# Kernel optimization log

Hardware: AMD Instinct MI355X
Metric: run time of the kernel (lower is better)

The kernel has to match this reference:

```python
import jax, jax.numpy as jnp
import numpy as np
from math import sqrt

DIM = 1024
RANK = 64
B, T = 4, 4096

def _xavier(key, shape):
    fan_in, fan_out = shape[1], shape[0]
    limit = sqrt(6.0 / (fan_in + fan_out))
    return jax.random.uniform(key, shape, jnp.float32, -limit, limit)

def setup_inputs() -> dict:
    key = jax.random.key(0)
    kx, kq, kk, kv = jax.random.split(key, 4)
    return {
        "x": jax.random.normal(kx, (B, T, DIM), jnp.float32),
        "Q": _xavier(kq, (RANK, DIM)),
        "K": _xavier(kk, (RANK, DIM)),
        "VO": _xavier(kv, (DIM, DIM)),
    }

def reference(x, Q, K, VO):
    dim = x.shape[-1]
    # low-rank projections: [b, t, r]
    xq = jnp.einsum('btd,rd->btr', x, Q)
    xk = jnp.einsum('bue,re->bur', x, K)
    scores = jnp.einsum('btr,bur->btu', xq, xk) / sqrt(dim)
    attn = jax.nn.softmax(scores, axis=2)
    # attn @ x @ VO: contract with VO first (cheap [b,u,d]@[d,e]) then attn
    return jnp.einsum('btu,bue->bte', attn, x @ VO)
```

## Files before the change

kernel.cpp:

```cpp
#include <hip/hip_runtime.h>
#include <hip/hip_bf16.h>

#define BATCH 4
#define SEQ   4096
#define DIM   1024
#define RANK  64

typedef __attribute__((ext_vector_type(8))) short short8;
typedef __attribute__((ext_vector_type(4))) short short4v;
typedef __attribute__((ext_vector_type(4))) float f32x4;

#define MFMA16(a,b,c) __builtin_amdgcn_mfma_f32_16x16x32_bf16((a),(b),(c),0,0,0)

#define XQ_OFF 0
#define XK_OFF (BATCH*SEQ*RANK)
#define VT_OFF (2*BATCH*SEQ*RANK)
#define VT_END (VT_OFF + BATCH*DIM*SEQ)
#define P_OFF  ((size_t)VT_END)
#define P_LEN  ((size_t)BATCH*SEQ*SEQ)

__device__ __forceinline__ short f2b(float f) {
    __hip_bfloat16 h = __float2bfloat16(f);
    short s; __builtin_memcpy(&s, &h, sizeof(short));
    return s;
}
__device__ __forceinline__ float b2f(short s) {
    __hip_bfloat16 h; __builtin_memcpy(&h, &s, sizeof(short));
    return __bfloat162float(h);
}
__device__ __forceinline__ short8 cvt8(const float* __restrict__ p) {
    const float4 f0 = *reinterpret_cast<const float4*>(p);
    const float4 f1 = *reinterpret_cast<const float4*>(p + 4);
    short8 r;
    r[0]=f2b(f0.x); r[1]=f2b(f0.y); r[2]=f2b(f0.z); r[3]=f2b(f0.w);
    r[4]=f2b(f1.x); r[5]=f2b(f1.y); r[6]=f2b(f1.z); r[7]=f2b(f1.w);
    return r;
}
__device__ __forceinline__ void gld16(const short* g, short* l) {
    __builtin_amdgcn_global_load_lds(
        (const __attribute__((address_space(1))) void*)g,
        (__attribute__((address_space(3))) void*)l, 16, 0, 0);
}

__global__ __launch_bounds__(256) void lr_cvt(const float* __restrict__ x,
                                              const float* __restrict__ VO,
                                              const float* __restrict__ Qw,
                                              const float* __restrict__ Kw,
                                              short* __restrict__ xb,
                                              short* __restrict__ VOt,
                                              short* __restrict__ Wb)
{
    const int bid = blockIdx.x, tid = threadIdx.x;
    if (bid < 8192) {
        const size_t base = ((size_t)bid*256 + tid)*8;
        *reinterpret_cast<short8*>(xb + base) = cvt8(x + base);
    } else if (bid < 8448) {
        __shared__ short tr[64*68];
        const int bb = bid - 8192;
        const int dt = bb >> 4, et = bb & 15;
        const int d0 = dt*64, e0 = et*64;
        const int ein = tid & 63, din = tid >> 6;
        #pragma unroll
        for (int j = 0; j < 16; ++j) {
            const int dl = din + j*4;
            tr[ein*68 + dl] = f2b(VO[(size_t)(d0 + dl)*DIM + e0 + ein]);
        }
        __syncthreads();
        const int or_ = tid >> 4, oc = (tid & 15)*4;
        #pragma unroll
        for (int j = 0; j < 4; ++j) {
            const int el = or_ + j*16;
            short4v v;
            v[0]=tr[el*68+oc]; v[1]=tr[el*68+oc+1];
            v[2]=tr[el*68+oc+2]; v[3]=tr[el*68+oc+3];
            *reinterpret_cast<short4v*>(VOt + (size_t)(e0+el)*DIM + d0 + oc) = v;
        }
    } else {
        const int gid = (bid - 8448)*256 + tid;
        const int row = gid >> 7, c8 = (gid & 127)*8;
        const float* src = (row < 64 ? Qw + (size_t)row*DIM
                                     : Kw + (size_t)(row-64)*DIM) + c8;
        *reinterpret_cast<short8*>(Wb + (size_t)row*DIM + c8) = cvt8(src);
    }
}

__global__ __launch_bounds__(256, 4) void lr_proj2(const short* __restrict__ xb,
                                                   const short* __restrict__ Wb,
                                                   short* __restrict__ ws)
{
    __shared__ __align__(16) short As[128*64];
    __shared__ __align__(16) short Bs[128*64];
    const int t0 = blockIdx.x*128;
    const int tid = threadIdx.x, lane = tid & 63, w = tid >> 6;
    const int l15 = lane & 15, g = lane >> 4;
    const int wr = w >> 1, wc = w & 1;
    const short* Ab = xb + (size_t)t0*DIM;
    const short* Bb = Wb;
    const int srow = lane >> 3;
    const int skc  = ((lane & 7) ^ srow)*8;
    const int rx = l15 & 7;

    f32x4 acc[4][4] = {};
    #pragma unroll
    for (int j = 0; j < 4; ++j) {
        const int ch = 4*w + j, row = ch*8 + srow;
        gld16(Ab + (size_t)row*DIM + skc, &As[ch*512]);
        gld16(Bb + (size_t)row*DIM + skc, &Bs[ch*512]);
    }
    for (int kt = 0; kt < 16; ++kt) {
        __syncthreads();
        #pragma unroll
        for (int ks = 0; ks < 2; ++ks) {
            short8 af[4], bfr[4];
            #pragma unroll
            for (int mr = 0; mr < 4; ++mr)
                af[mr] = *reinterpret_cast<const short8*>(
                    &As[(wr*64 + mr*16 + l15)*64 + ((ks*4 + g) ^ rx)*8]);
            #pragma unroll
            for (int ct = 0; ct < 4; ++ct)
                bfr[ct] = *reinterpret_cast<const short8*>(
                    &Bs[(wc*64 + ct*16 + l15)*64 + ((ks*4 + g) ^ rx)*8]);
            #pragma unroll
            for (int mr = 0; mr < 4; ++mr)
                #pragma unroll
                for (int ct = 0; ct < 4; ++ct)
                    acc[mr][ct] = MFMA16(af[mr], bfr[ct], acc[mr][ct]);
        }
        if (kt < 15) {
            __syncthreads();
            const int k0 = (kt + 1)*64;
            #pragma unroll
            for (int j = 0; j < 4; ++j) {
                const int ch = 4*w + j, row = ch*8 + srow;
                gld16(Ab + (size_t)row*DIM + k0 + skc, &As[ch*512]);
                gld16(Bb + (size_t)row*DIM + k0 + skc, &Bs[ch*512]);
            }
        }
    }
    short* xqp = ws + XQ_OFF;
    short* xkp = ws + XK_OFF;
    #pragma unroll
    for (int mr = 0; mr < 4; ++mr)
        #pragma unroll
        for (int rr = 0; rr < 4; ++rr) {
            const int t = t0 + wr*64 + mr*16 + g*4 + rr;
            #pragma unroll
            for (int ct = 0; ct < 4; ++ct) {
                const int r = wc*64 + ct*16 + l15;
                const short v = f2b(acc[mr][ct][rr]);
                if (r < RANK) xqp[(size_t)t*RANK + r] = v;
                else          xkp[(size_t)t*RANK + r - RANK] = v;
            }
        }
}

__global__ __launch_bounds__(256, 4) void lr_vgemm2(const short* __restrict__ VOt,
                                                    const short* __restrict__ xb,
                                                    short* __restrict__ vT)
{
    __shared__ __align__(16) short As[128*64];
    __shared__ __align__(16) short Bs[128*64];
    const int i = blockIdx.x;
    const int etile = i & 7, j = i >> 3;
    const int ut = j & 31, b = j >> 5;
    const int e0 = etile*128, u0 = ut*128;
    const int tid = threadIdx.x, lane = tid & 63, w = tid >> 6;
    const int l15 = lane & 15, g = lane >> 4;
    const int wr = w >> 1, wc = w & 1;
    const short* Ab = VOt + (size_t)e0*DIM;
    const short* Bb = xb + ((size_t)(b*SEQ) + u0)*DIM;
    const int srow = lane >> 3;
    const int skc  = ((lane & 7) ^ srow)*8;
    const int rx = l15 & 7;

    f32x4 acc[4][4] = {};
    #pragma unroll
    for (int jj = 0; jj < 4; ++jj) {
        const int ch = 4*w + jj, row = ch*8 + srow;
        gld16(Ab + (size_t)row*DIM + skc, &As[ch*512]);
        gld16(Bb + (size_t)row*DIM + skc, &Bs[ch*512]);
    }
    for (int kt = 0; kt < 16; ++kt) {
        __syncthreads();
        #pragma unroll
        for (int ks = 0; ks < 2; ++ks) {
            short8 af[4], bfr[4];
            #pragma unroll
            for (int mr = 0; mr < 4; ++mr)
                af[mr] = *reinterpret_cast<const short8*>(
                    &As[(wr*64 + mr*16 + l15)*64 + ((ks*4 + g) ^ rx)*8]);
            #pragma unroll
            for (int ct = 0; ct < 4; ++ct)
                bfr[ct] = *reinterpret_cast<const short8*>(
                    &Bs[(wc*64 + ct*16 + l15)*64 + ((ks*4 + g) ^ rx)*8]);
            #pragma unroll
            for (int mr = 0; mr < 4; ++mr)
                #pragma unroll
                for (int ct = 0; ct < 4; ++ct)
                    acc[mr][ct] = MFMA16(af[mr], bfr[ct], acc[mr][ct]);
        }
        if (kt < 15) {
            __syncthreads();
            const int k0 = (kt + 1)*64;
            #pragma unroll
            for (int jj = 0; jj < 4; ++jj) {
                const int ch = 4*w + jj, row = ch*8 + srow;
                gld16(Ab + (size_t)row*DIM + k0 + skc, &As[ch*512]);
                gld16(Bb + (size_t)row*DIM + k0 + skc, &Bs[ch*512]);
            }
        }
    }
    #pragma unroll
    for (int mr = 0; mr < 4; ++mr)
        #pragma unroll
        for (int rr = 0; rr < 4; ++rr) {
            const int e = e0 + wr*64 + mr*16 + g*4 + rr;
            short* orow = vT + ((size_t)(b*DIM) + e)*SEQ + u0 + wc*64;
            #pragma unroll
            for (int ct = 0; ct < 4; ++ct)
                orow[ct*16 + l15] = f2b(acc[mr][ct][rr]);
        }
}

__global__ __launch_bounds__(256, 4) void lr_pexp(const short* __restrict__ ws,
                                                  short* __restrict__ P,
                                                  float* __restrict__ ps)
{
    __shared__ __align__(16) short ptile[128*136];
    __shared__ float sred[4][128];
    const int i = blockIdx.x;
    const int qt = i >> 5, ut = i & 31;
    const int b = qt >> 5;
    const int tid = threadIdx.x, lane = tid & 63, w = tid >> 6;
    const int l15 = lane & 15, g = lane >> 4;
    const float cl = 0.045084220f;
    const int q0 = qt*128;

    const short* xqb = ws + XQ_OFF + (size_t)q0*RANK;
    const short* xkb = ws + XK_OFF + ((size_t)(b*SEQ) + ut*128)*RANK;

    f32x4 acc[2][8] = {};
    #pragma unroll
    for (int ks = 0; ks < 2; ++ks) {
        short8 ak[2], bq[8];
        #pragma unroll
        for (int mr = 0; mr < 2; ++mr)
            ak[mr] = *reinterpret_cast<const short8*>(
                xkb + (size_t)(32*w + mr*16 + l15)*RANK + ks*32 + g*8);
        #pragma unroll
        for (int ct = 0; ct < 8; ++ct)
            bq[ct] = *reinterpret_cast<const short8*>(
                xqb + (size_t)(ct*16 + l15)*RANK + ks*32 + g*8);
        #pragma unroll
        for (int mr = 0; mr < 2; ++mr)
            #pragma unroll
            for (int ct = 0; ct < 8; ++ct)
                acc[mr][ct] = MFMA16(ak[mr], bq[ct], acc[mr][ct]);
    }
    float s[8] = {0.f,0.f,0.f,0.f,0.f,0.f,0.f,0.f};
    #pragma unroll
    for (int mr = 0; mr < 2; ++mr)
        #pragma unroll
        for (int ct = 0; ct < 8; ++ct) {
            short4v pk;
            #pragma unroll
            for (int r = 0; r < 4; ++r) {
                const short pb = f2b(__builtin_amdgcn_exp2f(acc[mr][ct][r]*cl));
                pk[r] = pb;
                s[ct] += b2f(pb);
            }
            *reinterpret_cast<short4v*>(
                &ptile[(ct*16 + l15)*136 + 32*w + mr*16 + g*4]) = pk;
        }
    #pragma unroll
    for (int ct = 0; ct < 8; ++ct) {
        s[ct] += __shfl_xor(s[ct], 16);
        s[ct] += __shfl_xor(s[ct], 32);
    }
    if (g == 0) {
        #pragma unroll
        for (int ct = 0; ct < 8; ++ct) sred[w][ct*16 + l15] = s[ct];
    }
    __syncthreads();
    #pragma unroll
    for (int j = 0; j < 8; ++j) {
        const int id = tid + 256*j;
        const int row = id >> 4, seg = id & 15;
        const uint4 v = *reinterpret_cast<const uint4*>(&ptile[row*136 + seg*8]);
        *reinterpret_cast<uint4*>(
            P + (size_t)(q0 + row)*SEQ + ut*128 + seg*8) = v;
    }
    if (tid < 128)
        ps[(size_t)(q0 + tid)*32 + ut] =
            sred[0][tid] + sred[1][tid] + sred[2][tid] + sred[3][tid];
}

__global__ __launch_bounds__(256) void lr_psum(const float* __restrict__ ps,
                                               float* __restrict__ linv)
{
    const int gq = blockIdx.x*256 + threadIdx.x;
    const float* p = ps + (size_t)gq*32;
    float s = 0.f;
    #pragma unroll
    for (int j = 0; j < 32; ++j) s += p[j];
    linv[gq] = 1.0f / s;
}

__global__ __launch_bounds__(256, 4) void lr_pv(const short* __restrict__ P,
                                                const short* __restrict__ vT,
                                                const float* __restrict__ linv,
                                                float* __restrict__ out)
{
    __shared__ __align__(16) short As[128*64];
    __shared__ __align__(16) short Bs[128*64];
    const int i = blockIdx.x;
    const int qlo = i & 7, j = i >> 3;
    const int nt = j & 7, qhi = j >> 3;
    const int qt = qhi*8 + qlo;
    const int q0 = qt*128, d0 = nt*128, b = qt >> 5;
    const int tid = threadIdx.x, lane = tid & 63, w = tid >> 6;
    const int l15 = lane & 15, g = lane >> 4;
    const int wr = w >> 1, wc = w & 1;

    const short* Ab = P + (size_t)q0*SEQ;
    const short* Bb = vT + ((size_t)(b*DIM) + d0)*SEQ;
    const int srow = lane >> 3;
    const int skc  = ((lane & 7) ^ srow)*8;
    const int rx = l15 & 7;

    f32x4 acc[4][4] = {};
    #pragma unroll
    for (int jj = 0; jj < 4; ++jj) {
        const int ch = 4*w + jj, row = ch*8 + srow;
        gld16(Ab + (size_t)row*SEQ + skc, &As[ch*512]);
        gld16(Bb + (size_t)row*SEQ + skc, &Bs[ch*512]);
    }
    for (int kt = 0; kt < 64; ++kt) {
        __syncthreads();
        #pragma unroll
        for (int ks = 0; ks < 2; ++ks) {
            short8 af[4], bfr[4];
            #pragma unroll
            for (int mr = 0; mr < 4; ++mr)
                af[mr] = *reinterpret_cast<const short8*>(
                    &As[(wr*64 + mr*16 + l15)*64 + ((ks*4 + g) ^ rx)*8]);
            #pragma unroll
            for (int ct = 0; ct < 4; ++ct)
                bfr[ct] = *reinterpret_cast<const short8*>(
                    &Bs[(wc*64 + ct*16 + l15)*64 + ((ks*4 + g) ^ rx)*8]);
            #pragma unroll
            for (int mr = 0; mr < 4; ++mr)
                #pragma unroll
                for (int ct = 0; ct < 4; ++ct)
                    acc[mr][ct] = MFMA16(af[mr], bfr[ct], acc[mr][ct]);
        }
        if (kt < 63) {
            __syncthreads();
            const int k0 = (kt + 1)*64;
            #pragma unroll
            for (int jj = 0; jj < 4; ++jj) {
                const int ch = 4*w + jj, row = ch*8 + srow;
                gld16(Ab + (size_t)row*SEQ + k0 + skc, &As[ch*512]);
                gld16(Bb + (size_t)row*SEQ + k0 + skc, &Bs[ch*512]);
            }
        }
    }
    #pragma unroll
    for (int mr = 0; mr < 4; ++mr)
        #pragma unroll
        for (int rr = 0; rr < 4; ++rr) {
            const int q = q0 + wr*64 + mr*16 + g*4 + rr;
            const float sc = linv[q];
            float* rp = out + (size_t)q*DIM + d0 + wc*64;
            #pragma unroll
            for (int ct = 0; ct < 4; ++ct)
                rp[ct*16 + l15] = acc[mr][ct][rr]*sc;
        }
}

__global__ __launch_bounds__(256) void lr_proj(const float* __restrict__ x,
                                               const float* __restrict__ Qw,
                                               const float* __restrict__ Kw,
                                               short* __restrict__ ws)
{
    __shared__ __align__(16) short ldsB[64*40];
    const int i = blockIdx.x;
    const int ttile = i & 63, b = i >> 6;
    const int tid = threadIdx.x, lane = tid & 63, w = tid >> 6;
    const int l15 = lane & 15, g = lane >> 4;
    const int t0 = ttile * 64;

    f32x4 acc[2][4] = {};
    for (int e0 = 0; e0 < DIM; e0 += 32) {
        const int tr = tid >> 2, seg = tid & 3;
        const float* px = x + (size_t)(b*SEQ + t0 + tr)*DIM + e0 + seg*8;
        const float4 f0 = *reinterpret_cast<const float4*>(px);
        const float4 f1 = *reinterpret_cast<const float4*>(px + 4);
        __syncthreads();
        {
            short* d = &ldsB[tr*40 + seg*8];
            d[0]=f2b(f0.x); d[1]=f2b(f0.y); d[2]=f2b(f0.z); d[3]=f2b(f0.w);
            d[4]=f2b(f1.x); d[5]=f2b(f1.y); d[6]=f2b(f1.z); d[7]=f2b(f1.w);
        }
        __syncthreads();
        #pragma unroll
        for (int mr = 0; mr < 2; ++mr) {
            const int r = 32*w + mr*16 + l15;
            const float* wp = (r < RANK ? Qw + (size_t)r*DIM
                                        : Kw + (size_t)(r - RANK)*DIM) + e0 + g*8;
            const short8 a = cvt8(wp);
            #pragma unroll
            for (int ct = 0; ct < 4; ++ct) {
                const short8 bb = *reinterpret_cast<const short8*>(
                    &ldsB[(ct*16 + l15)*40 + g*8]);
                acc[mr][ct] = MFMA16(a, bb, acc[mr][ct]);
            }
        }
    }
    short* xqp = ws + XQ_OFF;
    short* xkp = ws + XK_OFF;
    #pragma unroll
    for (int mr = 0; mr < 2; ++mr) {
        const int rb = 32*w + mr*16 + g*4;
        short* base = (rb < RANK) ? (xqp + rb) : (xkp + (rb - RANK));
        #pragma unroll
        for (int ct = 0; ct < 4; ++ct) {
            const int t = t0 + ct*16 + l15;
            short4v pk;
            pk[0]=f2b(acc[mr][ct][0]); pk[1]=f2b(acc[mr][ct][1]);
            pk[2]=f2b(acc[mr][ct][2]); pk[3]=f2b(acc[mr][ct][3]);
            *reinterpret_cast<short4v*>(base + (size_t)(b*SEQ + t)*RANK) = pk;
        }
    }
}

__global__ __launch_bounds__(256) void lr_vgemm(const float* __restrict__ x,
                                                const float* __restrict__ VO,
                                                short* __restrict__ ws)
{
    short* vT = ws + VT_OFF;
    __shared__ __align__(16) short ldsA[128*40];
    __shared__ __align__(16) short ldsB[128*40];
    const int i = blockIdx.x;
    const int dtile = i & 7, utile = (i >> 3) & 31, b = i >> 8;
    const int d0 = dtile*128, u0 = utile*128;
    const int tid = threadIdx.x, lane = tid & 63, w = tid >> 6;
    const int l15 = lane & 15, g = lane >> 4;
    const int wr = w >> 1, wc = w & 1;

    f32x4 acc[4][4] = {};
    for (int e0 = 0; e0 < DIM; e0 += 32) {
        const int dcol = tid & 127, erg = (tid >> 7)*16;
        float va[16];
        #pragma unroll
        for (int j = 0; j < 16; ++j)
            va[j] = VO[(size_t)(e0 + erg + j)*DIM + d0 + dcol];
        const int ur = tid >> 1, esg = (tid & 1)*16;
        const float* pb = x + (size_t)(b*SEQ + u0 + ur)*DIM + e0 + esg;
        float4 vb0 = reinterpret_cast<const float4*>(pb)[0];
        float4 vb1 = reinterpret_cast<const float4*>(pb)[1];
        float4 vb2 = reinterpret_cast<const float4*>(pb)[2];
        float4 vb3 = reinterpret_cast<const float4*>(pb)[3];
        __syncthreads();
        #pragma unroll
        for (int j = 0; j < 16; ++j) ldsA[dcol*40 + erg + j] = f2b(va[j]);
        {
            short* d = &ldsB[ur*40 + esg];
            d[0]=f2b(vb0.x); d[1]=f2b(vb0.y); d[2]=f2b(vb0.z); d[3]=f2b(vb0.w);
            d[4]=f2b(vb1.x); d[5]=f2b(vb1.y); d[6]=f2b(vb1.z); d[7]=f2b(vb1.w);
            d[8]=f2b(vb2.x); d[9]=f2b(vb2.y); d[10]=f2b(vb2.z); d[11]=f2b(vb2.w);
            d[12]=f2b(vb3.x); d[13]=f2b(vb3.y); d[14]=f2b(vb3.z); d[15]=f2b(vb3.w);
        }
        __syncthreads();
        short8 af[4], bfr[4];
        #pragma unroll
        for (int mr = 0; mr < 4; ++mr)
            af[mr] = *reinterpret_cast<const short8*>(
                &ldsA[(wr*64 + mr*16 + l15)*40 + g*8]);
        #pragma unroll
        for (int ct = 0; ct < 4; ++ct)
            bfr[ct] = *reinterpret_cast<const short8*>(
                &ldsB[(wc*64 + ct*16 + l15)*40 + g*8]);
        #pragma unroll
        for (int mr = 0; mr < 4; ++mr)
            #pragma unroll
            for (int ct = 0; ct < 4; ++ct)
                acc[mr][ct] = MFMA16(af[mr], bfr[ct], acc[mr][ct]);
    }
    #pragma unroll
    for (int mr = 0; mr < 4; ++mr)
        #pragma unroll
        for (int rr = 0; rr < 4; ++rr) {
            const int d = d0 + wr*64 + mr*16 + g*4 + rr;
            short* orow = vT + (size_t)(b*DIM + d)*SEQ + u0 + wc*64;
            #pragma unroll
            for (int ct = 0; ct < 4; ++ct)
                orow[ct*16 + l15] = f2b(acc[mr][ct][rr]);
        }
}

__global__ __launch_bounds__(256) void lr_stats(const short* __restrict__ ws,
                                                float* __restrict__ pm,
                                                float* __restrict__ pl)
{
    const short* xq = ws + XQ_OFF;
    const short* xk = ws + XK_OFF;
    const int i = blockIdx.x;
    const int us = i & 3, qtile = (i >> 2) & 63, b = i >> 8;
    const int tid = threadIdx.x, lane = tid & 63, w = tid >> 6;
    const int l15 = lane & 15, g = lane >> 4;
    const float cl = 0.045084220f;

    short8 qb0, qb1;
    {
        const short* p = xq + (size_t)(b*SEQ + qtile*64 + 16*w + l15)*RANK + g*8;
        qb0 = *reinterpret_cast<const short8*>(p);
        qb1 = *reinterpret_cast<const short8*>(p + 32);
    }
    const short* kb = xk + (size_t)b*SEQ*RANK;

    float m = -3.0e38f, l = 0.f;
    for (int it = 0; it < 16; ++it) {
        const int ub = us*1024 + it*64;
        f32x4 S[4];
        #pragma unroll
        for (int t = 0; t < 4; ++t) {
            const short* kp = kb + (size_t)(ub + 16*t + l15)*RANK + g*8;
            const short8 a0 = *reinterpret_cast<const short8*>(kp);
            const short8 a1 = *reinterpret_cast<const short8*>(kp + 32);
            f32x4 z = {};
            z = MFMA16(a0, qb0, z);
            z = MFMA16(a1, qb1, z);
            S[t] = z;
        }
        float mt = S[0][0];
        #pragma unroll
        for (int t = 0; t < 4; ++t)
            #pragma unroll
            for (int r = 0; r < 4; ++r) mt = fmaxf(mt, S[t][r]);
        const float mn = fmaxf(m, mt);
        l *= __builtin_amdgcn_exp2f((m - mn)*cl);
        const float mc = mn*cl;
        #pragma unroll
        for (int t = 0; t < 4; ++t)
            #pragma unroll
            for (int r = 0; r < 4; ++r)
                l += __builtin_amdgcn_exp2f(__builtin_fmaf(S[t][r], cl, -mc));
        m = mn;
    }
    #pragma unroll
    for (int mask = 16; mask <= 32; mask <<= 1) {
        const float mo = __shfl_xor(m, mask), lo = __shfl_xor(l, mask);
        const float mn = fmaxf(m, mo);
        l = l*__builtin_amdgcn_exp2f((m - mn)*cl)
          + lo*__builtin_amdgcn_exp2f((mo - mn)*cl);
        m = mn;
    }
    if (g == 0) {
        const int idx = (b*SEQ + qtile*64 + 16*w + l15)*4 + us;
        pm[idx] = m; pl[idx] = l;
    }
}

__global__ __launch_bounds__(256, 4) void lr_flash(const short* __restrict__ ws,
                                                   const float* __restrict__ pm,
                                                   const float* __restrict__ pl,
                                                   float* __restrict__ out)
{
    const short* xq = ws + XQ_OFF;
    const short* xk = ws + XK_OFF;
    const short* vT = ws + VT_OFF;
    __shared__ __align__(16) short vlds[128*64];
    __shared__ __align__(16) short plds[32*64];
    const int i = blockIdx.x;
    const int xcd = i & 7, slot = i >> 3;
    const int combo = xcd + 8*(slot >> 6);
    const int qtile = slot & 63;
    const int b = combo >> 2, dch = combo & 3;
    const int tid = threadIdx.x, lane = tid & 63, w = tid >> 6;
    const int l15 = lane & 15, g = lane >> 4;
    const float cl = 0.045084220f;

    float mC;
    {
        const int base = (b*SEQ + qtile*64 + 16*w + l15)*4;
        const float m0 = pm[base+0], m1 = pm[base+1];
        const float m2 = pm[base+2], m3 = pm[base+3];
        const float mm = fmaxf(fmaxf(m0, m1), fmaxf(m2, m3));
        const float l = pl[base+0]*__builtin_amdgcn_exp2f((m0-mm)*cl)
                      + pl[base+1]*__builtin_amdgcn_exp2f((m1-mm)*cl)
                      + pl[base+2]*__builtin_amdgcn_exp2f((m2-mm)*cl)
                      + pl[base+3]*__builtin_amdgcn_exp2f((m3-mm)*cl);
        mC = -(mm*cl + __builtin_amdgcn_logf(l));
    }
    short8 qb0, qb1;
    {
        const short* p = xq + (size_t)(b*SEQ + qtile*64 + 16*w + l15)*RANK + g*8;
        qb0 = *reinterpret_cast<const short8*>(p);
        qb1 = *reinterpret_cast<const short8*>(p + 32);
    }
    const short* vbase = vT + ((size_t)b*DIM + dch*256)*SEQ;
    const short* kr = xk + (size_t)b*SEQ*RANK + l15*RANK + g*8;
    const int r7 = l15 >> 1;
    const int st_dst = (tid >> 3)*64 + (((tid & 7) ^ ((tid >> 3) & 7))*8);
    const int st_src = (tid >> 2)*SEQ + (tid & 3)*8;
    const int a_base = r7*64 + ((((l15 & 1)*4 + g) ^ r7)*8);
    const int b_base = (32*w + r7)*64 + ((((l15 & 1)*4 + g) ^ r7)*8);
    const int chv = (l15 & 1)*4 + (g >> 1);
    const int pw0 = (8*w + r7)*64 + ((chv ^ r7)*8)       + (g & 1)*4;
    const int pw1 = (8*w + r7)*64 + (((chv + 2) ^ r7)*8) + (g & 1)*4;

    uint4 sreg[4];
    #pragma unroll
    for (int c = 0; c < 4; ++c)
        sreg[c] = *reinterpret_cast<const uint4*>(vbase + st_src + (size_t)c*64*SEQ);
    #pragma unroll
    for (int c = 0; c < 4; ++c)
        *reinterpret_cast<uint4*>(&vlds[st_dst + 2048*c]) = sreg[c];

    f32x4 O[16] = {};
    for (int ub = 0; ub < SEQ; ub += 32) {
        const bool more = (ub + 32 < SEQ);
        if (more) {
            #pragma unroll
            for (int c = 0; c < 4; ++c)
                sreg[c] = *reinterpret_cast<const uint4*>(
                    vbase + st_src + ub + 32 + (size_t)c*64*SEQ);
        }
        #pragma unroll
        for (int t = 0; t < 2; ++t) {
            const short* kp = kr + (size_t)(ub + 16*t)*RANK;
            const short8 a0 = *reinterpret_cast<const short8*>(kp);
            const short8 a1 = *reinterpret_cast<const short8*>(kp + 32);
            f32x4 z = {};
            z = MFMA16(a0, qb0, z);
            z = MFMA16(a1, qb1, z);
            short4v pk;
            #pragma unroll
            for (int r = 0; r < 4; ++r)
                pk[r] = f2b(__builtin_amdgcn_exp2f(__builtin_fmaf(z[r], cl, mC)));
            *reinterpret_cast<short4v*>(&plds[t ? pw1 : pw0]) = pk;
        }
        __syncthreads();
        short8 pa[4];
        #pragma unroll
        for (int qt = 0; qt < 4; ++qt)
            pa[qt] = *reinterpret_cast<const short8*>(&plds[a_base + qt*512]);
        #pragma unroll
        for (int dt = 0; dt < 4; ++dt) {
            const short8 vf = *reinterpret_cast<const short8*>(&vlds[b_base + dt*512]);
            #pragma unroll
            for (int qt = 0; qt < 4; ++qt)
                O[qt*4 + dt] = MFMA16(pa[qt], vf, O[qt*4 + dt]);
        }
        __syncthreads();
        if (more) {
            #pragma unroll
            for (int c = 0; c < 4; ++c)
                *reinterpret_cast<uint4*>(&vlds[st_dst + 2048*c]) = sreg[c];
        }
    }
    #pragma unroll
    for (int qt = 0; qt < 4; ++qt)
        #pragma unroll
        for (int rr = 0; rr < 4; ++rr) {
            const int q = qtile*64 + qt*16 + g*4 + rr;
            float* rowp = out + (size_t)(b*SEQ + q)*DIM + dch*256 + 64*w;
            #pragma unroll
            for (int dt = 0; dt < 4; ++dt)
                rowp[dt*16 + l15] = O[qt*4 + dt][rr];
        }
}

extern "C" void kernel_launch(void* const* d_in, const int* in_sizes, int n_in,
                              void* d_out, int out_size, void* d_ws, size_t ws_size,
                              hipStream_t stream) {
    const float* x  = (const float*)d_in[0];
    const float* Q  = (const float*)d_in[1];
    const float* K  = (const float*)d_in[2];
    const float* VO = (const float*)d_in[3];
    float* out = (float*)d_out;
    short* ws = (short*)d_ws;

    const size_t need = (P_OFF + P_LEN)*2 + (size_t)(BATCH*SEQ)*(32 + 1)*4;
    if (ws_size >= need) {
        short* Pb  = ws + P_OFF;
        short* xb  = Pb;
        short* VOt = Pb + (size_t)BATCH*SEQ*DIM;
        short* Wb  = VOt + (size_t)DIM*DIM;
        float* ps  = (float*)(ws + P_OFF + P_LEN);
        float* linv = ps + (size_t)BATCH*SEQ*32;
        lr_cvt   <<<dim3(8512), dim3(256), 0, stream>>>(x, VO, Q, K, xb, VOt, Wb);
        lr_proj2 <<<dim3(128),  dim3(256), 0, stream>>>(xb, Wb, ws);
        lr_vgemm2<<<dim3(1024), dim3(256), 0, stream>>>(VOt, xb, ws + VT_OFF);
        lr_pexp  <<<dim3(4096), dim3(256), 0, stream>>>(ws, Pb, ps);
        lr_psum  <<<dim3(64),   dim3(256), 0, stream>>>(ps, linv);
        lr_pv    <<<dim3(1024), dim3(256), 0, stream>>>(Pb, ws + VT_OFF, linv, out);
    } else {
        float* pm = (float*)(ws + VT_END);
        float* pl = pm + BATCH*SEQ*4;
        lr_proj <<<dim3(256),  dim3(256), 0, stream>>>(x, Q, K, ws);
        lr_stats<<<dim3(1024), dim3(256), 0, stream>>>(ws, pm, pl);
        lr_vgemm<<<dim3(1024), dim3(256), 0, stream>>>(x, VO, ws);
        lr_flash<<<dim3(1024), dim3(256), 0, stream>>>(ws, pm, pl, out);
    }
}
```

Measured before the change: 263.8 us.

## Add 256x256-tile 8-wave PV GEMM with interleaved prefetch and LDS double buffering

Replaces the 128x128-tile P@V kernel with a 256x256 tile computed by 512 threads (8 waves), using 128 KB of dynamic LDS double-buffered across K steps. Global-to-LDS loads for the next K tile are split into quarters and interleaved between MFMA phases, with s_setprio raised around the MFMA clusters, to overlap memory and compute. The larger tile halves the global traffic per flop and cuts the grid to 256 blocks, at the cost of one block per CU (256 CUs) and high register pressure from 32 accumulator tiles. It falls back to the old kernel if the LDS attribute cannot be set.

```diff
diff --git a/kernel.cpp b/kernel.cpp
--- a/kernel.cpp
+++ b/kernel.cpp
@@ -306,6 +306,205 @@
     linv[gq] = 1.0f / s;
 }
 
+__global__ __launch_bounds__(512, 2) void lr_pv8(const short* __restrict__ P,
+                                                 const short* __restrict__ vT,
+                                                 const float* __restrict__ linv,
+                                                 float* __restrict__ out)
+{
+    extern __shared__ __align__(16) short lds[];
+    short* As = lds;
+    short* Bs = lds + 32768;
+    const int bid = blockIdx.x;
+    const int qt = (bid & 7)*8 + (bid >> 5);
+    const int nt = (bid >> 3) & 3;
+    const int q0 = qt*256, d0 = nt*256, b = qt >> 4;
+    const int tid = threadIdx.x, lane = tid & 63, w = tid >> 6;
+    const int wr = w >> 2, wc = w & 3;
+    const int l15 = lane & 15, g = lane >> 4;
+    const int rx = l15 & 7;
+
+    const short* Ab = P + (size_t)q0*SEQ;
+    const short* Bb = vT + ((size_t)(b*DIM) + d0)*SEQ;
+
+    int aA0[2], aA1[2], aB0[2], aB1[2];
+    int dA0[2], dA1[2], dB0[2], dB1[2];
+    #pragma unroll
+    for (int j = 0; j < 2; ++j) {
+        const int s = tid + 512*j;
+        const int cl = s >> 6, v = s & 63;
+        const int vr = v >> 3, vk = ((v & 7) ^ vr)*8;
+        const int cA0 = (cl < 8) ? cl : cl + 8;
+        const int cA1 = cA0 + 8;
+        const int cB0 = ((cl >> 2) << 3) + (cl & 3);
+        const int cB1 = cB0 + 4;
+        aA0[j] = (cA0*8 + vr)*SEQ + vk;  dA0[j] = cA0*512 + v*8;
+        aA1[j] = (cA1*8 + vr)*SEQ + vk;  dA1[j] = cA1*512 + v*8;
+        aB0[j] = (cB0*8 + vr)*SEQ + vk;  dB0[j] = cB0*512 + v*8;
+        aB1[j] = (cB1*8 + vr)*SEQ + vk;  dB1[j] = cB1*512 + v*8;
+    }
+
+    f32x4 acc[8][4] = {};
+    short8 af[4][2], bf[4][2];
+
+    #pragma unroll
+    for (int j = 0; j < 2; ++j) gld16(Ab + aA0[j], &As[dA0[j]]);
+    #pragma unroll
+    for (int j = 0; j < 2; ++j) gld16(Bb + aB0[j], &Bs[dB0[j]]);
+    #pragma unroll
+    for (int j = 0; j < 2; ++j) gld16(Bb + aB1[j], &Bs[dB1[j]]);
+    #pragma unroll
+    for (int j = 0; j < 2; ++j) gld16(Ab + aA1[j], &As[dA1[j]]);
+    asm volatile("s_waitcnt vmcnt(4)" ::: "memory");
+    __builtin_amdgcn_s_barrier();
+    __builtin_amdgcn_sched_barrier(0);
+
+    for (int kt = 0; kt < 63; ++kt) {
+        const int buf  = (kt & 1) ? 16384 : 0;
+        const int nbuf = 16384 - buf;
+        const int kn = (kt + 1)*64;
+        const int arow = buf + (wr*128 + l15)*64;
+        const int brow = buf + (wc*64 + l15)*64;
+        #pragma unroll
+        for (int mf = 0; mf < 4; ++mf)
+            #pragma unroll
+            for (int ks = 0; ks < 2; ++ks)
+                af[mf][ks] = *reinterpret_cast<const short8*>(
+                    &As[arow + mf*1024 + ((ks*4 + g) ^ rx)*8]);
+        #pragma unroll
+        for (int nf = 0; nf < 2; ++nf)
+            #pragma unroll
+            for (int ks = 0; ks < 2; ++ks)
+                bf[nf][ks] = *reinterpret_cast<const short8*>(
+                    &Bs[brow + nf*1024 + ((ks*4 + g) ^ rx)*8]);
+        #pragma unroll
+        for (int j = 0; j < 2; ++j) gld16(Ab + aA0[j] + kn, &As[nbuf + dA0[j]]);
+        __builtin_amdgcn_s_barrier();
+        asm volatile("s_waitcnt lgkmcnt(0)" ::: "memory");
+        __builtin_amdgcn_sched_barrier(0);
+        __builtin_amdgcn_s_setprio(1);
+        #pragma unroll
+        for (int mf = 0; mf < 4; ++mf)
+            #pragma unroll
+            for (int nf = 0; nf < 2; ++nf)
+                #pragma unroll
+                for (int ks = 0; ks < 2; ++ks)
+                    acc[mf][nf] = MFMA16(af[mf][ks], bf[nf][ks], acc[mf][nf]);
+        __builtin_amdgcn_s_setprio(0);
+        asm volatile("s_waitcnt vmcnt(4)" ::: "memory");
+        __builtin_amdgcn_s_barrier();
+        __builtin_amdgcn_sched_barrier(0);
+        #pragma unroll
+        for (int nf = 2; nf < 4; ++nf)
+            #pragma unroll
+            for (int ks = 0; ks < 2; ++ks)
+                bf[nf][ks] = *reinterpret_cast<const short8*>(
+                    &Bs[brow + nf*1024 + ((ks*4 + g) ^ rx)*8]);
+        #pragma unroll
+        for (int j = 0; j < 2; ++j) gld16(Bb + aB0[j] + kn, &Bs[nbuf + dB0[j]]);
+        __builtin_amdgcn_s_barrier();
+        asm volatile("s_waitcnt lgkmcnt(0)" ::: "memory");
+        __builtin_amdgcn_sched_barrier(0);
+        __builtin_amdgcn_s_setprio(1);
+        #pragma unroll
+        for (int mf = 0; mf < 4; ++mf)
+            #pragma unroll
+            for (int nf = 2; nf < 4; ++nf)
+                #pragma unroll
+                for (int ks = 0; ks < 2; ++ks)
+                    acc[mf][nf] = MFMA16(af[mf][ks], bf[nf][ks], acc[mf][nf]);
+        __builtin_amdgcn_s_setprio(0);
+        asm volatile("s_waitcnt vmcnt(4)" ::: "memory");
+        __builtin_amdgcn_s_barrier();
+        __builtin_amdgcn_sched_barrier(0);
+        #pragma unroll
+        for (int mf = 0; mf < 4; ++mf)
+            #pragma unroll
+            for (int ks = 0; ks < 2; ++ks)
+                af[mf][ks] = *reinterpret_cast<const short8*>(
+                    &As[arow + 4096 + mf*1024 + ((ks*4 + g) ^ rx)*8]);
+        #pragma unroll
+        for (int j = 0; j < 2; ++j) gld16(Bb + aB1[j] + kn, &Bs[nbuf + dB1[j]]);
+        __builtin_amdgcn_s_barrier();
+        asm volatile("s_waitcnt lgkmcnt(0)" ::: "memory");
+        __builtin_amdgcn_sched_barrier(0);
+        __builtin_amdgcn_s_setprio(1);
+        #pragma unroll
+        for (int mf = 0; mf < 4; ++mf)
+            #pragma unroll
+            for (int nf = 0; nf < 2; ++nf)
+                #pragma unroll
+                for (int ks = 0; ks < 2; ++ks)
+                    acc[mf+4][nf] = MFMA16(af[mf][ks], bf[nf][ks], acc[mf+4][nf]);
+        __builtin_amdgcn_s_setprio(0);
+        __builtin_amdgcn_s_barrier();
+        __builtin_amdgcn_sched_barrier(0);
+        #pragma unroll
+        for (int j = 0; j < 2; ++j) gld16(Ab + aA1[j] + kn, &As[nbuf + dA1[j]]);
+        __builtin_amdgcn_s_setprio(1);
+        #pragma unroll
+        for (int mf = 0; mf < 4; ++mf)
+            #pragma unroll
+            for (int nf = 2; nf < 4; ++nf)
+                #pragma unroll
+                for (int ks = 0; ks < 2; ++ks)
+                    acc[mf+4][nf] = MFMA16(af[mf][ks], bf[nf][ks], acc[mf+4][nf]);
+        __builtin_amdgcn_s_setprio(0);
+        asm volatile("s_waitcnt vmcnt(4)" ::: "memory");
+        __builtin_amdgcn_s_barrier();
+        __builtin_amdgcn_sched_barrier(0);
+    }
+    asm volatile("s_waitcnt vmcnt(0)" ::: "memory");
+    __builtin_amdgcn_s_barrier();
+    __builtin_amdgcn_sched_barrier(0);
+    {
+        const int arow = 16384 + (wr*128 + l15)*64;
+        const int brow = 16384 + (wc*64 + l15)*64;
+        #pragma unroll
+        for (int mf = 0; mf < 4; ++mf)
+            #pragma unroll
+            for (int ks = 0; ks < 2; ++ks)
+                af[mf][ks] = *reinterpret_cast<const short8*>(
+                    &As[arow + mf*1024 + ((ks*4 + g) ^ rx)*8]);
+        #pragma unroll
+        for (int nf = 0; nf < 4; ++nf)
+            #pragma unroll
+            for (int ks = 0; ks < 2; ++ks)
+                bf[nf][ks] = *reinterpret_cast<const short8*>(
+                    &Bs[brow + nf*1024 + ((ks*4 + g) ^ rx)*8]);
+        #pragma unroll
+        for (int mf = 0; mf < 4; ++mf)
+            #pragma unroll
+            for (int nf = 0; nf < 4; ++nf)
+                #pragma unroll
+                for (int ks = 0; ks < 2; ++ks)
+                    acc[mf][nf] = MFMA16(af[mf][ks], bf[nf][ks], acc[mf][nf]);
+        #pragma unroll
+        for (int mf = 0; mf < 4; ++mf)
+            #pragma unroll
+            for (int ks = 0; ks < 2; ++ks)
+                af[mf][ks] = *reinterpret_cast<const short8*>(
+                    &As[arow + 4096 + mf*1024 + ((ks*4 + g) ^ rx)*8]);
+        #pragma unroll
+        for (int mf = 0; mf < 4; ++mf)
+            #pragma unroll
+            for (int nf = 0; nf < 4; ++nf)
+                #pragma unroll
+                for (int ks = 0; ks < 2; ++ks)
+                    acc[mf+4][nf] = MFMA16(af[mf][ks], bf[nf][ks], acc[mf+4][nf]);
+    }
+    #pragma unroll
+    for (int mf = 0; mf < 8; ++mf)
+        #pragma unroll
+        for (int rr = 0; rr < 4; ++rr) {
+            const int q = q0 + wr*128 + mf*16 + g*4 + rr;
+            const float sc = linv[q];
+            float* rp = out + (size_t)q*DIM + d0 + wc*64;
+            #pragma unroll
+            for (int nf = 0; nf < 4; ++nf)
+                rp[nf*16 + l15] = acc[mf][nf][rr]*sc;
+        }
+}
+
 __global__ __launch_bounds__(256, 4) void lr_pv(const short* __restrict__ P,
                                                 const short* __restrict__ vT,
                                                 const float* __restrict__ linv,
@@ -695,7 +894,13 @@
         lr_vgemm2<<<dim3(1024), dim3(256), 0, stream>>>(VOt, xb, ws + VT_OFF);
         lr_pexp  <<<dim3(4096), dim3(256), 0, stream>>>(ws, Pb, ps);
         lr_psum  <<<dim3(64),   dim3(256), 0, stream>>>(ps, linv);
-        lr_pv    <<<dim3(1024), dim3(256), 0, stream>>>(Pb, ws + VT_OFF, linv, out);
+        const hipError_t e = hipFuncSetAttribute(
+            reinterpret_cast<const void*>(lr_pv8),
+            hipFuncAttributeMaxDynamicSharedMemorySize, 131072);
+        if (e == hipSuccess)
+            lr_pv8<<<dim3(256), dim3(512), 131072, stream>>>(Pb, ws + VT_OFF, linv, out);
+        else
+            lr_pv <<<dim3(1024), dim3(256), 0, stream>>>(Pb, ws + VT_OFF, linv, out);
     } else {
         float* pm = (float*)(ws + VT_END);
         float* pl = pm + BATCH*SEQ*4;
```

After: 246.4 us. 6.6% less time.
